# Optimization experiments

Hardware: AMD Instinct MI355X
Metric: run time of the kernel (lower is better)

The kernel has to match this reference:

```python
import jax, jax.numpy as jnp
import numpy as np

EMBED_DIMS = 192
NUM_HEADS = 6
WH, WW = 7, 7
N_TOK = WH * WW
B_WIN = 4096


def _rpe_index(Wh, Ww):
    coords = np.array([[x, y] for x in range(Ww) for y in range(Wh)])  # [N,2]
    d = coords[None, :, :] - coords[:, None, :]                        # [N,N,2]
    idx = (d[:, :, 0] + Ww - 1) * (2 * Ww - 1) + (d[:, :, 1] + Wh - 1)
    return idx.T  # transpose(0,1) as in the torch code


def setup_inputs() -> dict:
    key = jax.random.key(0)
    ks = jax.random.split(key, 6)
    C = EMBED_DIMS
    return {
        "x": jax.random.normal(ks[0], (B_WIN, N_TOK, C), dtype=jnp.float32),
        "qkv_w": jax.random.normal(ks[1], (3 * C, C), dtype=jnp.float32) * 0.02,
        "qkv_b": jax.random.normal(ks[2], (3 * C,), dtype=jnp.float32) * 0.02,
        "proj_w": jax.random.normal(ks[3], (C, C), dtype=jnp.float32) * 0.02,
        "proj_b": jax.random.normal(ks[4], (C,), dtype=jnp.float32) * 0.02,
        "rpe_table": jax.random.normal(ks[5], ((2 * WH - 1) * (2 * WW - 1), NUM_HEADS), dtype=jnp.float32),
        "rpe_idx": jnp.asarray(_rpe_index(WH, WW), dtype=jnp.int32),
    }


def reference(x, qkv_w, qkv_b, proj_w, proj_b, rpe_table, rpe_idx):
    B, N, C = x.shape
    H = NUM_HEADS
    hd = C // H
    scale = hd ** -0.5
    # qkv projection: torch Linear is x @ W.T + b
    qkv = x @ qkv_w.T + qkv_b                      # [B, N, 3C]
    qkv = qkv.reshape(B, N, 3, H, hd).transpose(2, 0, 3, 1, 4)  # [3, B, H, N, hd]
    q, k, v = qkv[0] * scale, qkv[1], qkv[2]
    attn = jnp.einsum("bhnd,bhmd->bhnm", q, k)     # [B, H, N, N]
    # relative position bias gather: table[idx] -> [N, N, H] -> [H, N, N]
    bias = rpe_table[rpe_idx].transpose(2, 0, 1)
    attn = jax.nn.softmax(attn + bias, axis=-1)
    out = jnp.einsum("bhnm,bhmd->bhnd", attn, v)   # [B, H, N, hd]
    out = out.transpose(0, 2, 1, 3).reshape(B, N, C)
    return out @ proj_w.T + proj_b
```

## Files before the change

kernel.cpp:

```cpp
#include <hip/hip_runtime.h>
#include <stdint.h>

#define NWIN 4096
#define NTOK 49
#define CDIM 192
#define NH   6
#define HD   32

typedef __attribute__((ext_vector_type(8))) short short8;
typedef __attribute__((ext_vector_type(4))) float floatx4;
typedef unsigned short ushort_t;
typedef unsigned int uint32;

#define XS_S 200
#define QK_S 136
#define P_S  72
#define VT_S 72

#define OFF_REG0 0
#define OFF_QKS  9800
#define OFF_PB   16464
#define OFF_VT   19992
#define LDS_TOT  24600

__device__ __forceinline__ ushort_t f2bf(float f) {
    uint32 u = __float_as_uint(f);
    u += 0x7fffu + ((u >> 16) & 1u);
    return (ushort_t)(u >> 16);
}

__global__ void wmsa_prologue(const float* __restrict__ qkv_w,
                              const float* __restrict__ proj_w,
                              const float* __restrict__ rpe_table,
                              const int*   __restrict__ rpe_idx,
                              ushort_t* __restrict__ qkv_wb,
                              ushort_t* __restrict__ proj_wb,
                              float* __restrict__ biasws)
{
    int i = blockIdx.x * 256 + threadIdx.x;
    if (i < 110592) {
        qkv_wb[i] = f2bf(qkv_w[i]);
    } else if (i < 147456) {
        proj_wb[i - 110592] = f2bf(proj_w[i - 110592]);
    } else if (i < 147456 + NH * NTOK * 64) {
        int r = i - 147456;
        int h = r / (NTOK * 64);
        int rem = r - h * (NTOK * 64);
        int n = rem >> 6, m = rem & 63;
        biasws[r] = (m < NTOK) ? rpe_table[rpe_idx[n * NTOK + m] * NH + h] : 0.f;
    }
}

__global__ __launch_bounds__(256)
void wmsa_mfma(const float* __restrict__ x,
               const ushort_t* __restrict__ qkv_wb,
               const float* __restrict__ qkv_b,
               const ushort_t* __restrict__ proj_wb,
               const float* __restrict__ proj_b,
               const float* __restrict__ biasws,
               float* __restrict__ out)
{
    __shared__ alignas(16) ushort_t lds[LDS_TOT];
    ushort_t* const reg0 = lds + OFF_REG0;
    ushort_t* const qks  = lds + OFF_QKS;
    ushort_t* const Pb   = lds + OFF_PB;
    ushort_t* const Vt   = lds + OFF_VT;

    const int b    = blockIdx.x;
    const int t    = threadIdx.x;
    const int w    = t >> 6;
    const int lane = t & 63;
    const int quad = lane >> 4;
    const int c    = lane & 15;
    const float scale = 0.17677669529663687f;

    const float* xb = x + (size_t)b * (NTOK * CDIM);

    for (int i = t; i < (NTOK * CDIM) / 4; i += 256) {
        int e = i * 4;
        int n = e / CDIM, d = e - n * CDIM;
        float4 v = *(const float4*)(xb + e);
        ushort_t* p = &reg0[n * XS_S + d];
        p[0] = f2bf(v.x); p[1] = f2bf(v.y); p[2] = f2bf(v.z); p[3] = f2bf(v.w);
    }
    __syncthreads();

    short8 afr[4][6];
    #pragma unroll
    for (int mt = 0; mt < 4; ++mt) {
        int row = mt * 16 + c;
        #pragma unroll
        for (int ks = 0; ks < 6; ++ks)
            afr[mt][ks] = *(const short8*)&reg0[row * XS_S + ks * 32 + quad * 8];
    }

    for (int pass = 0; pass < 3; ++pass) {
        for (int nt = w; nt < 12; nt += 4) {
            int s_idx = nt >> 2;
            int rem   = nt & 3;
            int hh    = rem >> 1;
            int half  = rem & 1;
            int jrow  = s_idx * CDIM + (2 * pass + hh) * HD + half * 16 + c;
            const ushort_t* bp = qkv_wb + jrow * CDIM + quad * 8;

            floatx4 z = {0.f, 0.f, 0.f, 0.f};
            floatx4 acc[4];
            #pragma unroll
            for (int mt = 0; mt < 4; ++mt) acc[mt] = z;

            #pragma unroll
            for (int ks = 0; ks < 6; ++ks) {
                short8 bf = *(const short8*)(bp + ks * 32);
                #pragma unroll
                for (int mt = 0; mt < 4; ++mt)
                    acc[mt] = __builtin_amdgcn_mfma_f32_16x16x32_bf16(
                        afr[mt][ks], bf, acc[mt], 0, 0, 0);
            }

            float bias = qkv_b[jrow];
            if (s_idx == 2) {
                int vrow = hh * HD + half * 16 + c;
                #pragma unroll
                for (int mt = 0; mt < 4; ++mt) {
                    #pragma unroll
                    for (int r = 0; r < 4; ++r) {
                        int n = mt * 16 + quad * 4 + r;
                        Vt[vrow * VT_S + n] =
                            (n < NTOK) ? f2bf(acc[mt][r] + bias) : (ushort_t)0;
                    }
                }
            } else {
                float mul = (s_idx == 0) ? scale : 1.f;
                int ecol  = hh * 64 + s_idx * 32 + half * 16 + c;
                #pragma unroll
                for (int mt = 0; mt < 4; ++mt) {
                    #pragma unroll
                    for (int r = 0; r < 4; ++r) {
                        int n = mt * 16 + quad * 4 + r;
                        if (n < NTOK)
                            qks[n * QK_S + ecol] = f2bf((acc[mt][r] + bias) * mul);
                    }
                }
            }
        }
        __syncthreads();

        for (int hh = 0; hh < 2; ++hh) {
            int h = pass * 2 + hh;

            short8 aq = *(const short8*)&qks[(w * 16 + c) * QK_S + hh * 64 + quad * 8];
            floatx4 sacc[4];
            #pragma unroll
            for (int nt = 0; nt < 4; ++nt) {
                short8 bk = *(const short8*)&qks[(nt * 16 + c) * QK_S + hh * 64 + 32 + quad * 8];
                floatx4 z = {0.f, 0.f, 0.f, 0.f};
                sacc[nt] = __builtin_amdgcn_mfma_f32_16x16x32_bf16(aq, bk, z, 0, 0, 0);
            }

            const float* bpb = biasws + h * (NTOK * 64);
            #pragma unroll
            for (int r = 0; r < 4; ++r) {
                int n  = w * 16 + quad * 4 + r;
                int nc = (n < NTOK) ? n : (NTOK - 1);
                float sv[4];
                #pragma unroll
                for (int nt = 0; nt < 4; ++nt) {
                    int col = nt * 16 + c;
                    float bias = bpb[nc * 64 + col];
                    sv[nt] = (col < NTOK) ? (sacc[nt][r] + bias) : -1e30f;
                }
                float m0 = fmaxf(fmaxf(sv[0], sv[1]), fmaxf(sv[2], sv[3]));
                m0 = fmaxf(m0, __shfl_xor(m0, 1));
                m0 = fmaxf(m0, __shfl_xor(m0, 2));
                m0 = fmaxf(m0, __shfl_xor(m0, 4));
                m0 = fmaxf(m0, __shfl_xor(m0, 8));
                float ex[4], s0 = 0.f;
                #pragma unroll
                for (int nt = 0; nt < 4; ++nt) { ex[nt] = __expf(sv[nt] - m0); s0 += ex[nt]; }
                s0 += __shfl_xor(s0, 1);
                s0 += __shfl_xor(s0, 2);
                s0 += __shfl_xor(s0, 4);
                s0 += __shfl_xor(s0, 8);
                float inv = 1.f / s0;
                if (n < NTOK) {
                    #pragma unroll
                    for (int nt = 0; nt < 4; ++nt)
                        Pb[n * P_S + nt * 16 + c] = f2bf(ex[nt] * inv);
                }
            }

            floatx4 z2 = {0.f, 0.f, 0.f, 0.f};
            floatx4 oacc[2]; oacc[0] = z2; oacc[1] = z2;
            #pragma unroll
            for (int ks = 0; ks < 2; ++ks) {
                short8 ap = *(const short8*)&Pb[(w * 16 + c) * P_S + ks * 32 + quad * 8];
                #pragma unroll
                for (int nt = 0; nt < 2; ++nt) {
                    short8 bv = *(const short8*)&Vt[(hh * HD + nt * 16 + c) * VT_S + ks * 32 + quad * 8];
                    oacc[nt] = __builtin_amdgcn_mfma_f32_16x16x32_bf16(ap, bv, oacc[nt], 0, 0, 0);
                }
            }
            #pragma unroll
            for (int nt = 0; nt < 2; ++nt) {
                #pragma unroll
                for (int r = 0; r < 4; ++r) {
                    int n = w * 16 + quad * 4 + r;
                    if (n < NTOK)
                        reg0[n * XS_S + h * HD + nt * 16 + c] = f2bf(oacc[nt][r]);
                }
            }
        }
        __syncthreads();
    }

    short8 aof[4][6];
    #pragma unroll
    for (int mt = 0; mt < 4; ++mt) {
        int row = mt * 16 + c;
        #pragma unroll
        for (int ks = 0; ks < 6; ++ks)
            aof[mt][ks] = *(const short8*)&reg0[row * XS_S + ks * 32 + quad * 8];
    }
    for (int nt = w; nt < 12; nt += 4) {
        int j = nt * 16 + c;
        const ushort_t* bp = proj_wb + j * CDIM + quad * 8;
        floatx4 z = {0.f, 0.f, 0.f, 0.f};
        floatx4 acc[4];
        #pragma unroll
        for (int mt = 0; mt < 4; ++mt) acc[mt] = z;
        #pragma unroll
        for (int ks = 0; ks < 6; ++ks) {
            short8 bf = *(const short8*)(bp + ks * 32);
            #pragma unroll
            for (int mt = 0; mt < 4; ++mt)
                acc[mt] = __builtin_amdgcn_mfma_f32_16x16x32_bf16(
                    aof[mt][ks], bf, acc[mt], 0, 0, 0);
        }
        float pb = proj_b[j];
        #pragma unroll
        for (int mt = 0; mt < 4; ++mt) {
            #pragma unroll
            for (int r = 0; r < 4; ++r) {
                int n = mt * 16 + quad * 4 + r;
                if (n < NTOK)
                    out[((size_t)b * NTOK + n) * CDIM + j] = acc[mt][r] + pb;
            }
        }
    }
}

extern "C" void kernel_launch(void* const* d_in, const int* in_sizes, int n_in,
                              void* d_out, int out_size, void* d_ws, size_t ws_size,
                              hipStream_t stream)
{
    const float* x      = (const float*)d_in[0];
    const float* qkv_w  = (const float*)d_in[1];
    const float* qkv_b  = (const float*)d_in[2];
    const float* proj_w = (const float*)d_in[3];
    const float* proj_b = (const float*)d_in[4];
    const float* rpe_t  = (const float*)d_in[5];
    const int*   rpe_i  = (const int*)d_in[6];
    float*       o      = (float*)d_out;

    ushort_t* qkv_wb  = (ushort_t*)d_ws;
    ushort_t* proj_wb = qkv_wb + 110592;
    float*    biasws  = (float*)((char*)d_ws + (110592 + 36864) * sizeof(ushort_t));

    int tot = 147456 + NH * NTOK * 64;
    wmsa_prologue<<<dim3((tot + 255) / 256), dim3(256), 0, stream>>>(
        qkv_w, proj_w, rpe_t, rpe_i, qkv_wb, proj_wb, biasws);
    wmsa_mfma<<<dim3(NWIN), dim3(256), 0, stream>>>(
        x, qkv_wb, qkv_b, proj_wb, proj_b, biasws, o);
}
```

Before: 555.0 us.

## Restructure QKV and projection loops to stream A fragments and hold attention outputs in registers

The QKV projection now has each wave compute its fixed Q, K and V tiles together, loading the x fragments per k-step from LDS instead of holding all 24 in registers. The per-head attention outputs are accumulated in registers across the three passes and written to LDS once at the end. This removes per-pass writes and one barrier, and the projection GEMM also streams its A fragments. The goal is lower register pressure and fewer LDS round-trips and syncs, at the cost of more LDS reads for the A operand and 48 extra accumulator registers held for out_acc.

```diff
diff --git a/kernel.cpp b/kernel.cpp
--- a/kernel.cpp
+++ b/kernel.cpp
@@ -17,7 +17,7 @@
 #define P_S  72
 #define VT_S 72
 
-#define OFF_REG0 0
+#define OFF_XS   0
 #define OFF_QKS  9800
 #define OFF_PB   16464
 #define OFF_VT   19992
@@ -61,10 +61,10 @@
                float* __restrict__ out)
 {
     __shared__ alignas(16) ushort_t lds[LDS_TOT];
-    ushort_t* const reg0 = lds + OFF_REG0;
-    ushort_t* const qks  = lds + OFF_QKS;
-    ushort_t* const Pb   = lds + OFF_PB;
-    ushort_t* const Vt   = lds + OFF_VT;
+    ushort_t* const xs  = lds + OFF_XS;
+    ushort_t* const qks = lds + OFF_QKS;
+    ushort_t* const Pb  = lds + OFF_PB;
+    ushort_t* const Vt  = lds + OFF_VT;
 
     const int b    = blockIdx.x;
     const int t    = threadIdx.x;
@@ -80,81 +80,72 @@
         int e = i * 4;
         int n = e / CDIM, d = e - n * CDIM;
         float4 v = *(const float4*)(xb + e);
-        ushort_t* p = &reg0[n * XS_S + d];
+        ushort_t* p = &xs[n * XS_S + d];
         p[0] = f2bf(v.x); p[1] = f2bf(v.y); p[2] = f2bf(v.z); p[3] = f2bf(v.w);
     }
     __syncthreads();
 
-    short8 afr[4][6];
-    #pragma unroll
-    for (int mt = 0; mt < 4; ++mt) {
-        int row = mt * 16 + c;
-        #pragma unroll
-        for (int ks = 0; ks < 6; ++ks)
-            afr[mt][ks] = *(const short8*)&reg0[row * XS_S + ks * 32 + quad * 8];
-    }
-
+    floatx4 out_acc[NH][2];
+    const floatx4 zf = {0.f, 0.f, 0.f, 0.f};
+    #pragma unroll
+    for (int h = 0; h < NH; ++h) { out_acc[h][0] = zf; out_acc[h][1] = zf; }
+
+    const int hh_w   = w >> 1;
+    const int half_w = w & 1;
+    const int jcol   = hh_w * 64 + half_w * 16 + c;
+
+    #pragma unroll
     for (int pass = 0; pass < 3; ++pass) {
-        for (int nt = w; nt < 12; nt += 4) {
-            int s_idx = nt >> 2;
-            int rem   = nt & 3;
-            int hh    = rem >> 1;
-            int half  = rem & 1;
-            int jrow  = s_idx * CDIM + (2 * pass + hh) * HD + half * 16 + c;
-            const ushort_t* bp = qkv_wb + jrow * CDIM + quad * 8;
-
-            floatx4 z = {0.f, 0.f, 0.f, 0.f};
-            floatx4 acc[4];
-            #pragma unroll
-            for (int mt = 0; mt < 4; ++mt) acc[mt] = z;
-
-            #pragma unroll
-            for (int ks = 0; ks < 6; ++ks) {
-                short8 bf = *(const short8*)(bp + ks * 32);
+        const int jbase = (2 * pass + hh_w) * HD + half_w * 16 + c;
+        floatx4 acc[3][4];
+        #pragma unroll
+        for (int s = 0; s < 3; ++s)
+            #pragma unroll
+            for (int mt = 0; mt < 4; ++mt) acc[s][mt] = zf;
+
+        #pragma unroll
+        for (int ks = 0; ks < 6; ++ks) {
+            short8 a4[4];
+            #pragma unroll
+            for (int mt = 0; mt < 4; ++mt)
+                a4[mt] = *(const short8*)&xs[(mt * 16 + c) * XS_S + ks * 32 + quad * 8];
+            #pragma unroll
+            for (int s = 0; s < 3; ++s) {
+                short8 bf = *(const short8*)&qkv_wb[(s * CDIM + jbase) * CDIM + ks * 32 + quad * 8];
                 #pragma unroll
                 for (int mt = 0; mt < 4; ++mt)
-                    acc[mt] = __builtin_amdgcn_mfma_f32_16x16x32_bf16(
-                        afr[mt][ks], bf, acc[mt], 0, 0, 0);
-            }
-
-            float bias = qkv_b[jrow];
-            if (s_idx == 2) {
-                int vrow = hh * HD + half * 16 + c;
-                #pragma unroll
-                for (int mt = 0; mt < 4; ++mt) {
-                    #pragma unroll
-                    for (int r = 0; r < 4; ++r) {
-                        int n = mt * 16 + quad * 4 + r;
-                        Vt[vrow * VT_S + n] =
-                            (n < NTOK) ? f2bf(acc[mt][r] + bias) : (ushort_t)0;
-                    }
-                }
-            } else {
-                float mul = (s_idx == 0) ? scale : 1.f;
-                int ecol  = hh * 64 + s_idx * 32 + half * 16 + c;
-                #pragma unroll
-                for (int mt = 0; mt < 4; ++mt) {
-                    #pragma unroll
-                    for (int r = 0; r < 4; ++r) {
-                        int n = mt * 16 + quad * 4 + r;
-                        if (n < NTOK)
-                            qks[n * QK_S + ecol] = f2bf((acc[mt][r] + bias) * mul);
-                    }
-                }
+                    acc[s][mt] = __builtin_amdgcn_mfma_f32_16x16x32_bf16(
+                        a4[mt], bf, acc[s][mt], 0, 0, 0);
+            }
+        }
+        float bq = qkv_b[jbase];
+        float bk = qkv_b[CDIM + jbase];
+        float bv = qkv_b[2 * CDIM + jbase];
+        #pragma unroll
+        for (int mt = 0; mt < 4; ++mt) {
+            #pragma unroll
+            for (int r = 0; r < 4; ++r) {
+                int n = mt * 16 + quad * 4 + r;
+                if (n < NTOK) {
+                    qks[n * QK_S + jcol]      = f2bf((acc[0][mt][r] + bq) * scale);
+                    qks[n * QK_S + jcol + 32] = f2bf(acc[1][mt][r] + bk);
+                }
+                Vt[(w * 16 + c) * VT_S + n] =
+                    (n < NTOK) ? f2bf(acc[2][mt][r] + bv) : (ushort_t)0;
             }
         }
         __syncthreads();
 
+        #pragma unroll
         for (int hh = 0; hh < 2; ++hh) {
-            int h = pass * 2 + hh;
+            const int h = pass * 2 + hh;
 
             short8 aq = *(const short8*)&qks[(w * 16 + c) * QK_S + hh * 64 + quad * 8];
             floatx4 sacc[4];
             #pragma unroll
             for (int nt = 0; nt < 4; ++nt) {
-                short8 bk = *(const short8*)&qks[(nt * 16 + c) * QK_S + hh * 64 + 32 + quad * 8];
-                floatx4 z = {0.f, 0.f, 0.f, 0.f};
-                sacc[nt] = __builtin_amdgcn_mfma_f32_16x16x32_bf16(aq, bk, z, 0, 0, 0);
+                short8 bk8 = *(const short8*)&qks[(nt * 16 + c) * QK_S + hh * 64 + 32 + quad * 8];
+                sacc[nt] = __builtin_amdgcn_mfma_f32_16x16x32_bf16(aq, bk8, zf, 0, 0, 0);
             }
 
             const float* bpb = biasws + h * (NTOK * 64);
@@ -189,63 +180,66 @@
                 }
             }
 
-            floatx4 z2 = {0.f, 0.f, 0.f, 0.f};
-            floatx4 oacc[2]; oacc[0] = z2; oacc[1] = z2;
-            #pragma unroll
-            for (int ks = 0; ks < 2; ++ks) {
-                short8 ap = *(const short8*)&Pb[(w * 16 + c) * P_S + ks * 32 + quad * 8];
+            #pragma unroll
+            for (int ks2 = 0; ks2 < 2; ++ks2) {
+                short8 ap = *(const short8*)&Pb[(w * 16 + c) * P_S + ks2 * 32 + quad * 8];
                 #pragma unroll
                 for (int nt = 0; nt < 2; ++nt) {
-                    short8 bv = *(const short8*)&Vt[(hh * HD + nt * 16 + c) * VT_S + ks * 32 + quad * 8];
-                    oacc[nt] = __builtin_amdgcn_mfma_f32_16x16x32_bf16(ap, bv, oacc[nt], 0, 0, 0);
-                }
-            }
-            #pragma unroll
-            for (int nt = 0; nt < 2; ++nt) {
-                #pragma unroll
-                for (int r = 0; r < 4; ++r) {
-                    int n = w * 16 + quad * 4 + r;
-                    if (n < NTOK)
-                        reg0[n * XS_S + h * HD + nt * 16 + c] = f2bf(oacc[nt][r]);
-                }
-            }
-        }
-        __syncthreads();
-    }
-
-    short8 aof[4][6];
-    #pragma unroll
-    for (int mt = 0; mt < 4; ++mt) {
-        int row = mt * 16 + c;
-        #pragma unroll
-        for (int ks = 0; ks < 6; ++ks)
-            aof[mt][ks] = *(const short8*)&reg0[row * XS_S + ks * 32 + quad * 8];
-    }
-    for (int nt = w; nt < 12; nt += 4) {
-        int j = nt * 16 + c;
-        const ushort_t* bp = proj_wb + j * CDIM + quad * 8;
-        floatx4 z = {0.f, 0.f, 0.f, 0.f};
-        floatx4 acc[4];
-        #pragma unroll
-        for (int mt = 0; mt < 4; ++mt) acc[mt] = z;
-        #pragma unroll
-        for (int ks = 0; ks < 6; ++ks) {
-            short8 bf = *(const short8*)(bp + ks * 32);
+                    short8 bv8 = *(const short8*)&Vt[(hh * HD + nt * 16 + c) * VT_S + ks2 * 32 + quad * 8];
+                    out_acc[h][nt] = __builtin_amdgcn_mfma_f32_16x16x32_bf16(
+                        ap, bv8, out_acc[h][nt], 0, 0, 0);
+                }
+            }
+        }
+        if (pass < 2) __syncthreads();
+    }
+
+    #pragma unroll
+    for (int h = 0; h < NH; ++h)
+        #pragma unroll
+        for (int nt = 0; nt < 2; ++nt)
+            #pragma unroll
+            for (int r = 0; r < 4; ++r) {
+                int n = w * 16 + quad * 4 + r;
+                if (n < NTOK)
+                    xs[n * XS_S + h * HD + nt * 16 + c] = f2bf(out_acc[h][nt][r]);
+            }
+    __syncthreads();
+
+    floatx4 pacc[3][4];
+    #pragma unroll
+    for (int tt = 0; tt < 3; ++tt)
+        #pragma unroll
+        for (int mt = 0; mt < 4; ++mt) pacc[tt][mt] = zf;
+
+    #pragma unroll
+    for (int ks = 0; ks < 6; ++ks) {
+        short8 a4[4];
+        #pragma unroll
+        for (int mt = 0; mt < 4; ++mt)
+            a4[mt] = *(const short8*)&xs[(mt * 16 + c) * XS_S + ks * 32 + quad * 8];
+        #pragma unroll
+        for (int tt = 0; tt < 3; ++tt) {
+            int j = (tt * 4 + w) * 16 + c;
+            short8 bf = *(const short8*)&proj_wb[j * CDIM + ks * 32 + quad * 8];
             #pragma unroll
             for (int mt = 0; mt < 4; ++mt)
-                acc[mt] = __builtin_amdgcn_mfma_f32_16x16x32_bf16(
-                    aof[mt][ks], bf, acc[mt], 0, 0, 0);
-        }
+                pacc[tt][mt] = __builtin_amdgcn_mfma_f32_16x16x32_bf16(
+                    a4[mt], bf, pacc[tt][mt], 0, 0, 0);
+        }
+    }
+    #pragma unroll
+    for (int tt = 0; tt < 3; ++tt) {
+        int j = (tt * 4 + w) * 16 + c;
         float pb = proj_b[j];
         #pragma unroll
-        for (int mt = 0; mt < 4; ++mt) {
+        for (int mt = 0; mt < 4; ++mt)
             #pragma unroll
             for (int r = 0; r < 4; ++r) {
                 int n = mt * 16 + quad * 4 + r;
                 if (n < NTOK)
-                    out[((size_t)b * NTOK + n) * CDIM + j] = acc[mt][r] + pb;
-            }
-        }
+                    out[((size_t)b * NTOK + n) * CDIM + j] = pacc[tt][mt][r] + pb;
+            }
     }
 }
 
```

New measurement: 593.7 us. 1.07x slower.
